# Performance work log

Measured on AMD Instinct MI355X. Metric: run time of the kernel, lower is better.

Reference implementation:

```python
import jax, jax.numpy as jnp
import numpy as np
from jax import lax

PART = 224   # PART_IMAGE_SIZE
PAD = 224    # PAD_SIZE
TOPN = 4
IOU_THRESH = 0.25
N_ANCHORS = 1614


def _conv(x, w, b, stride, pad):
    y = lax.conv_general_dilated(x, w, (stride, stride), [(pad, pad), (pad, pad)],
                                 dimension_numbers=('NCHW', 'OIHW', 'NCHW'))
    return y + b[None, :, None, None]


def _iou(box, boxes):
    # box [4], boxes [N,4] as (y0,x0,y1,x1)
    yy0 = jnp.maximum(box[0], boxes[:, 0]); xx0 = jnp.maximum(box[1], boxes[:, 1])
    yy1 = jnp.minimum(box[2], boxes[:, 2]); xx1 = jnp.minimum(box[3], boxes[:, 3])
    inter = jnp.clip(yy1 - yy0, 0.0) * jnp.clip(xx1 - xx0, 0.0)
    a = (box[2] - box[0]) * (box[3] - box[1])
    areas = (boxes[:, 2] - boxes[:, 0]) * (boxes[:, 3] - boxes[:, 1])
    return inter / (a + areas - inter)


def _nms(scores, boxes):
    # hard NMS keeping TOPN boxes; returns indices [TOPN]
    valid = jnp.ones(scores.shape, dtype=bool)
    idxs = []
    for _ in range(TOPN):
        i = jnp.argmax(jnp.where(valid, scores, -jnp.inf))
        idxs.append(i)
        valid = valid & (_iou(boxes[i], boxes) <= IOU_THRESH)
    return jnp.stack(idxs)


def _crop_resize(img, box):
    # img [3,Hp,Wp] padded image, box [4] float; bilinear, align_corners=True,
    # matching F.interpolate(x_pad[:, :, y0:y1, x0:x1], (PART, PART))
    Hp, Wp = img.shape[1], img.shape[2]
    def coords(c0, c1, L):
        t = jnp.arange(PART, dtype=img.dtype) / (PART - 1)
        c = c0 + (c1 - 1.0 - c0) * t          # absolute source coordinate
        cf = jnp.floor(c)
        lo = jnp.clip(cf.astype(jnp.int32), 0, L - 1)
        hi = jnp.clip(lo + 1, 0, L - 1)
        return lo, hi, c - cf
    yl, yh, wy = coords(box[0], box[2], Hp)
    xl, xh, wx = coords(box[1], box[3], Wp)
    g = lambda yi, xi: img[:, yi[:, None], xi[None, :]]   # [3,PART,PART]
    return ((1 - wy)[:, None] * ((1 - wx) * g(yl, xl) + wx * g(yl, xh))
            + wy[:, None] * ((1 - wx) * g(yh, xl) + wx * g(yh, xh)))


def setup_inputs() -> dict:
    key = jax.random.key(0)
    ks = jax.random.split(key, 20)
    x = jax.random.uniform(ks[0], (16, 3, 448, 448), dtype=jnp.float32)
    rpn_feature = jax.random.normal(ks[1], (16, 2048, 14, 14), dtype=jnp.float32)
    # valid boxes inside the padded 896x896 image
    y0 = jax.random.randint(ks[2], (N_ANCHORS,), 0, 560)
    x0 = jax.random.randint(ks[3], (N_ANCHORS,), 0, 560)
    h = jax.random.randint(ks[4], (N_ANCHORS,), 32, 336)
    w = jax.random.randint(ks[5], (N_ANCHORS,), 32, 336)
    anchors = jnp.stack([y0, x0, jnp.minimum(y0 + h, 896), jnp.minimum(x0 + w, 896)], axis=1).astype(jnp.int32)
    s = 0.02
    inp = {
        'x': x, 'rpn_feature': rpn_feature, 'anchors': anchors,
        'w_down1': jax.random.normal(ks[6], (128, 2048, 3, 3), jnp.float32) * s,
        'b_down1': jnp.zeros((128,), jnp.float32),
        'w_down2': jax.random.normal(ks[7], (128, 128, 3, 3), jnp.float32) * s,
        'b_down2': jnp.zeros((128,), jnp.float32),
        'w_down3': jax.random.normal(ks[8], (128, 128, 3, 3), jnp.float32) * s,
        'b_down3': jnp.zeros((128,), jnp.float32),
        'w_tidy1': jax.random.normal(ks[9], (6, 128, 1, 1), jnp.float32) * s,
        'b_tidy1': jnp.zeros((6,), jnp.float32),
        'w_tidy2': jax.random.normal(ks[10], (6, 128, 1, 1), jnp.float32) * s,
        'b_tidy2': jnp.zeros((6,), jnp.float32),
        'w_tidy3': jax.random.normal(ks[11], (9, 128, 1, 1), jnp.float32) * s,
        'b_tidy3': jnp.zeros((9,), jnp.float32),
    }
    return inp


def reference(x, rpn_feature, anchors,
              w_down1, b_down1, w_down2, b_down2, w_down3, b_down3,
              w_tidy1, b_tidy1, w_tidy2, b_tidy2, w_tidy3, b_tidy3):
    B = x.shape[0]
    # ProposalNet
    d1 = jax.nn.relu(_conv(rpn_feature, w_down1, b_down1, 1, 1))   # [B,128,14,14]
    d2 = jax.nn.relu(_conv(d1, w_down2, b_down2, 2, 1))            # [B,128,7,7]
    d3 = jax.nn.relu(_conv(d2, w_down3, b_down3, 2, 1))            # [B,128,4,4]
    t1 = _conv(d1, w_tidy1, b_tidy1, 1, 0).reshape(B, -1)
    t2 = _conv(d2, w_tidy2, b_tidy2, 1, 0).reshape(B, -1)
    t3 = _conv(d3, w_tidy3, b_tidy3, 1, 0).reshape(B, -1)
    rpn_score = jnp.concatenate([t1, t2, t3], axis=1)              # [B, 1614]
    boxes = anchors.astype(x.dtype)                                # [N,4]
    top_n_index = jax.vmap(lambda s: _nms(s, boxes))(rpn_score)    # [B,TOPN]
    top_n_prob = jnp.take_along_axis(rpn_score, top_n_index, axis=1)
    x_pad = jnp.pad(x, ((0, 0), (0, 0), (PAD, PAD), (PAD, PAD)))   # [B,3,896,896]
    sel_boxes = boxes[top_n_index]                                 # [B,TOPN,4]
    part_imgs = jax.vmap(lambda img, bxs: jax.vmap(lambda b: _crop_resize(img, b))(bxs))(x_pad, sel_boxes)
    # part_imgs: [B,TOPN,3,PART,PART]
    return rpn_score, top_n_index, top_n_prob, part_imgs
```

## Files before the change

kernel.cpp:

```cpp
#include <hip/hip_runtime.h>
#include <hip/hip_bf16.h>

#define NB 16
#define NA 1614
#define NBP (NB * 196 * 128)

typedef __bf16 bf16x8 __attribute__((ext_vector_type(8)));
typedef float f32x4 __attribute__((ext_vector_type(4)));

__device__ __forceinline__ unsigned short f2bf(float v) {
  unsigned u = __float_as_uint(v);
  unsigned r = (u + 0x7FFFu + ((u >> 16) & 1u)) >> 16;
  return (unsigned short)r;
}
__device__ __forceinline__ float bf2f(unsigned short s) {
  return __uint_as_float(((unsigned)s) << 16);
}

__global__ __launch_bounds__(256)
void prep(const float* __restrict__ w, const float* __restrict__ in,
          unsigned short* __restrict__ wTh, unsigned short* __restrict__ wTl,
          unsigned short* __restrict__ aTh, unsigned short* __restrict__ aTl) {
  __shared__ float s[32 * 201];
  const int bid = blockIdx.x;
  if (bid < 1024) {
    const int chunk = bid & 63, b = bid >> 6;
    const float* src = in + ((size_t)b * 2048 + chunk * 32) * 196;
#pragma unroll
    for (int r = 0; r < 7; r++) {
      int e = threadIdx.x + 256 * r;
      if (e < 1568) {
        int ic = e / 49, f = e - ic * 49;
        float4 v = ((const float4*)(src + (size_t)ic * 196))[f];
        float* d = s + ic * 201 + f * 4;
        d[0] = v.x; d[1] = v.y; d[2] = v.z; d[3] = v.w;
      }
    }
    __syncthreads();
    unsigned short* oh = aTh + (size_t)bid * (196 * 32);
    unsigned short* ol = aTl + (size_t)bid * (196 * 32);
#pragma unroll
    for (int r = 0; r < 4; r++) {
      int e = threadIdx.x + 256 * r;
      if (e < 784) {
        int pos = e >> 2, part = e & 3;
        unsigned short hv[8], lv[8];
#pragma unroll
        for (int j = 0; j < 8; j++) {
          float v = s[(part * 8 + j) * 201 + pos];
          unsigned short h = f2bf(v);
          hv[j] = h;
          lv[j] = f2bf(v - bf2f(h));
        }
        ((uint4*)oh)[e] = *(uint4*)hv;
        ((uint4*)ol)[e] = *(uint4*)lv;
      }
    }
  } else {
    int e = (bid - 1024) * 256 + threadIdx.x;
    if (e < 9 * 128 * 2048) {
      int tap = e / (128 * 2048);
      int rem = e - tap * (128 * 2048);
      int oc = rem >> 11, ic = rem & 2047;
      float v = w[((size_t)oc * 2048 + ic) * 9 + tap];
      unsigned short h = f2bf(v);
      wTh[e] = h;
      wTl[e] = f2bf(v - bf2f(h));
    }
  }
}

__global__ __launch_bounds__(256, 3)
void conv1_mfma(const unsigned short* __restrict__ aTh, const unsigned short* __restrict__ aTl,
                const unsigned short* __restrict__ wTh, const unsigned short* __restrict__ wTl,
                float* __restrict__ p1) {
  const int bid = blockIdx.x;
  const int b  = bid & 15;
  const int nh = (bid >> 4) & 1;
  const int kc = bid >> 5;
  const int tid = threadIdx.x;
  const int wid = tid >> 6, lane = tid & 63;
  const int wm = wid & 1, wn = wid >> 1;
  const int q = lane >> 4, ln = lane & 15;

  __shared__ unsigned short sAh[4 * 2048];
  __shared__ unsigned short sAl[4 * 2048];
  __shared__ unsigned short sBh[4 * 512];
  __shared__ unsigned short sBl[4 * 512];

  for (int e = tid; e < 4096; e += 256) {
    ((unsigned int*)sAh)[e] = 0u;
    ((unsigned int*)sAl)[e] = 0u;
  }

  int abase[7];
#pragma unroll
  for (int mf = 0; mf < 7; mf++) {
    int row = wm * 112 + mf * 16 + ln;
    int y = row / 14, x = row - y * 14;
    abase[mf] = ((row < 196) ? (y * 16 + x) : 0) * 8;
  }
  const int qoff = q * 2048;

  f32x4 acc[7][2];
#pragma unroll
  for (int mf = 0; mf < 7; mf++)
#pragma unroll
    for (int nf = 0; nf < 2; nf++) acc[mf][nf] = (f32x4){0.f, 0.f, 0.f, 0.f};

  const int boc = tid >> 2, bicq = tid & 3;
  const size_t bocbase = (size_t)(nh * 64 + boc) << 11;

  uint4 pvh, pvl;
  {
    size_t g = bocbase + kc * 128 + bicq * 8;
    pvh = *(const uint4*)(wTh + g);
    pvl = *(const uint4*)(wTl + g);
  }

  for (int it = 0; it < 36; it++) {
    const int ks = it / 9, tap = it - ks * 9;
    __syncthreads();
    *(uint4*)(sBh + bicq * 512 + boc * 8) = pvh;
    *(uint4*)(sBl + bicq * 512 + boc * 8) = pvl;
    if (tap == 0) {
      const uint4* gh = (const uint4*)(aTh + ((size_t)(b * 64 + kc * 4 + ks) * 196) * 32);
      const uint4* gl = (const uint4*)(aTl + ((size_t)(b * 64 + kc * 4 + ks) * 196) * 32);
#pragma unroll
      for (int r = 0; r < 4; r++) {
        int e = tid + 256 * r;
        if (e < 784) {
          int pos = e >> 2, part = e & 3;
          int py = pos / 14, px = pos - py * 14;
          int dst = part * 2048 + ((py + 1) * 16 + px + 1) * 8;
          *(uint4*)(sAh + dst) = gh[e];
          *(uint4*)(sAl + dst) = gl[e];
        }
      }
    }
    {
      const int nit = (it < 35) ? it + 1 : 35;
      const int ks2 = nit / 9, tap2 = nit - ks2 * 9;
      size_t g = (size_t)tap2 * (128 * 2048) + bocbase + kc * 128 + ks2 * 32 + bicq * 8;
      pvh = *(const uint4*)(wTh + g);
      pvl = *(const uint4*)(wTl + g);
    }
    __syncthreads();

    const int t8 = ((tap / 3) * 16 + (tap % 3)) * 8;
    bf16x8 bh[2], bl[2];
#pragma unroll
    for (int nf = 0; nf < 2; nf++) {
      const int bb = q * 512 + (wn * 32 + nf * 16 + ln) * 8;
      bh[nf] = *(const bf16x8*)(sBh + bb);
      bl[nf] = *(const bf16x8*)(sBl + bb);
    }
#pragma unroll
    for (int mf = 0; mf < 7; mf++) {
      bf16x8 ah = *(const bf16x8*)(sAh + qoff + abase[mf] + t8);
      bf16x8 al = *(const bf16x8*)(sAl + qoff + abase[mf] + t8);
#pragma unroll
      for (int nf = 0; nf < 2; nf++) {
        acc[mf][nf] = __builtin_amdgcn_mfma_f32_16x16x32_bf16(ah, bh[nf], acc[mf][nf], 0, 0, 0);
        acc[mf][nf] = __builtin_amdgcn_mfma_f32_16x16x32_bf16(al, bh[nf], acc[mf][nf], 0, 0, 0);
        acc[mf][nf] = __builtin_amdgcn_mfma_f32_16x16x32_bf16(ah, bl[nf], acc[mf][nf], 0, 0, 0);
      }
    }
  }

  float* pk = p1 + ((size_t)kc * NB + b) * 196 * 128;
#pragma unroll
  for (int mf = 0; mf < 7; mf++) {
    const int row0 = wm * 112 + mf * 16 + q * 4;
#pragma unroll
    for (int nf = 0; nf < 2; nf++) {
      const int oc = nh * 64 + wn * 32 + nf * 16 + ln;
#pragma unroll
      for (int r = 0; r < 4; r++) {
        const int row = row0 + r;
        if (row < 196) pk[(size_t)row * 128 + oc] = acc[mf][nf][r];
      }
    }
  }
}

__global__ __launch_bounds__(256)
void conv1_finish_p(const float* __restrict__ p1, const float* __restrict__ bias,
                    float* __restrict__ d1) {
  __shared__ float s[28 * 132];
  const int bid = blockIdx.x;
  const int pt = bid % 7, b = bid / 7;
  const int tid = threadIdx.x;
#pragma unroll
  for (int r = 0; r < 4; r++) {
    int u = tid + 256 * r;
    if (u < 896) {
      int pos = u >> 5, oc4 = u & 31;
      const float* base = p1 + ((size_t)(b * 196 + pt * 28 + pos)) * 128 + oc4 * 4;
      float4 sum = ((const float4*)bias)[oc4];
#pragma unroll
      for (int k = 0; k < 16; k++) {
        float4 v = *(const float4*)(base + (size_t)k * NBP);
        sum.x += v.x; sum.y += v.y; sum.z += v.z; sum.w += v.w;
      }
      sum.x = fmaxf(sum.x, 0.f); sum.y = fmaxf(sum.y, 0.f);
      sum.z = fmaxf(sum.z, 0.f); sum.w = fmaxf(sum.w, 0.f);
      *(float4*)(s + pos * 132 + oc4 * 4) = sum;
    }
  }
  __syncthreads();
#pragma unroll
  for (int r = 0; r < 4; r++) {
    int u = tid + 256 * r;
    if (u < 896) {
      int oc = u / 7, f = u - oc * 7;
      float4 v;
      v.x = s[(f * 4 + 0) * 132 + oc];
      v.y = s[(f * 4 + 1) * 132 + oc];
      v.z = s[(f * 4 + 2) * 132 + oc];
      v.w = s[(f * 4 + 3) * 132 + oc];
      *(float4*)(d1 + ((size_t)b * 128 + oc) * 196 + pt * 28 + f * 4) = v;
    }
  }
}

__global__ void conv2_part(const float* __restrict__ d1, const float* __restrict__ w,
                           float* __restrict__ p2) {
  const int bid = blockIdx.x;
  const int kc = bid & 3, oct = (bid >> 2) & 3, b = bid >> 4;
  const int ic0 = kc * 32, oc0 = oct * 32;
  const int tid = threadIdx.x;
  const int ocl = tid >> 3, rw = tid & 7;

  __shared__ float s_in[32 * 320];
  __shared__ float s_w[32 * 324];

#pragma unroll
  for (int r = 0; r < 32; r++) {
    const int e = tid + 256 * r;
    const int ch = e >> 8, idx = e & 255;
    const int tr = idx >> 4, tc = idx & 15;
    const int iy = tr - 1, ix = tc - 1;
    float v = 0.f;
    if ((unsigned)iy < 14u && (unsigned)ix < 14u)
      v = d1[((size_t)b * 128 + ic0 + ch) * 196 + iy * 14 + ix];
    s_in[ch * 320 + tr * 20 + tc] = v;
  }
#pragma unroll
  for (int r = 0; r < 36; r++) {
    const int e = tid + 256 * r;
    const int oc = e / 288, rem = e - oc * 288;
    const int ch = rem / 9, tap = rem - ch * 9;
    s_w[ch * 324 + tap * 36 + oc] =
        w[(size_t)(oc0 + oc) * 1152 + (size_t)ic0 * 9 + rem];
  }
  __syncthreads();

  if (rw < 7) {
    float acc[7] = {};
    for (int ic = 0; ic < 32; ic++) {
      const float* wrow = s_w + ic * 324 + ocl;
      const float* irow = s_in + ic * 320;
#pragma unroll
      for (int ky = 0; ky < 3; ky++) {
        const float* r = irow + (2 * rw + ky) * 20;
        const float4 f0 = *(const float4*)(r);
        const float4 f1 = *(const float4*)(r + 4);
        const float4 f2 = *(const float4*)(r + 8);
        const float4 f3 = *(const float4*)(r + 12);
        const float ev[8] = {f0.x, f0.z, f1.x, f1.z, f2.x, f2.z, f3.x, f3.z};
        const float od[7] = {f0.y, f0.w, f1.y, f1.w, f2.y, f2.w, f3.y};
        const float w0 = wrow[(ky * 3 + 0) * 36];
        const float w1 = wrow[(ky * 3 + 1) * 36];
        const float w2 = wrow[(ky * 3 + 2) * 36];
#pragma unroll
        for (int x = 0; x < 7; x++)
          acc[x] = fmaf(w0, ev[x], fmaf(w1, od[x], fmaf(w2, ev[x + 1], acc[x])));
      }
    }
    float* po = p2 + (((size_t)kc * NB + b) * 128 + oc0 + ocl) * 49 + rw * 7;
#pragma unroll
    for (int x = 0; x < 7; x++) po[x] = acc[x];
  }
}

__global__ void conv2_finish(const float* __restrict__ p2, const float* __restrict__ bias,
                             float* __restrict__ d2) {
  const int i = blockIdx.x * 256 + threadIdx.x;
  if (i >= NB * 128 * 49) return;
  const int oc = (i / 49) & 127;
  float s = bias[oc];
#pragma unroll
  for (int k = 0; k < 4; k++) s += p2[(size_t)k * (NB * 128 * 49) + i];
  d2[i] = fmaxf(s, 0.f);
}

__global__ void conv3_part(const float* __restrict__ d2, const float* __restrict__ w,
                           float* __restrict__ p3) {
  const int bid = blockIdx.x;
  const int kc = bid & 1, oct = (bid >> 1) & 7, b = bid >> 4;
  const int ic0 = kc * 64, oc0 = oct * 16;
  const int tid = threadIdx.x;
  const int oc = tid >> 4, p = tid & 15;
  const int y = p >> 2, x = p & 3;

  __shared__ float s_in[64 * 108];
  __shared__ float s_w[64 * 144];

#pragma unroll
  for (int r = 0; r < 21; r++) {
    const int e = tid + 256 * r;
    if (e < 64 * 81) {
      const int ch = e / 81, idx = e - ch * 81;
      const int tr = idx / 9, tc = idx - tr * 9;
      const int iy = tr - 1, ix = tc - 1;
      float v = 0.f;
      if ((unsigned)iy < 7u && (unsigned)ix < 7u)
        v = d2[((size_t)b * 128 + ic0 + ch) * 49 + iy * 7 + ix];
      s_in[ch * 108 + tr * 12 + tc] = v;
    }
  }
#pragma unroll
  for (int r = 0; r < 36; r++) {
    const int e = tid + 256 * r;
    const int o = e / 576, rem = e - o * 576;
    const int ch = rem / 9, tap = rem - ch * 9;
    s_w[ch * 144 + tap * 16 + o] =
        w[(size_t)(oc0 + o) * 1152 + (size_t)ic0 * 9 + rem];
  }
  __syncthreads();

  float acc = 0.f;
  for (int ic = 0; ic < 64; ic++) {
    const float* wrow = s_w + ic * 144 + oc;
    const float* irow = s_in + ic * 108 + 2 * y * 12 + 2 * x;
#pragma unroll
    for (int ky = 0; ky < 3; ky++)
#pragma unroll
      for (int kx = 0; kx < 3; kx++)
        acc = fmaf(wrow[(ky * 3 + kx) * 16], irow[ky * 12 + kx], acc);
  }
  p3[(((size_t)kc * NB + b) * 128 + oc0 + oc) * 16 + p] = acc;
}

__global__ __launch_bounds__(256, 1)
void score_nms(const float* __restrict__ d1, const float* __restrict__ d2,
               const float* __restrict__ p3, const float* __restrict__ bd3,
               const float* __restrict__ w1, const float* __restrict__ b1,
               const float* __restrict__ w2, const float* __restrict__ b2,
               const float* __restrict__ w3, const float* __restrict__ b3,
               const int* __restrict__ anchors, float* __restrict__ score,
               float* __restrict__ out_idx, float* __restrict__ out_prob,
               float* __restrict__ sel) {
  __shared__ float s_in[32 * 200];
  __shared__ float s_w[21 * 128];
  __shared__ float s_b[21];
  __shared__ float s_sc[NA];
  __shared__ float s_bx[NA * 4];
  __shared__ float r_s[256];
  __shared__ int r_i[256];
  const int b = blockIdx.x, tid = threadIdx.x;

  for (int i = tid; i < 768; i += 256) s_w[i] = w1[i];
  for (int i = tid; i < 768; i += 256) s_w[768 + i] = w2[i];
  for (int i = tid; i < 1152; i += 256) s_w[1536 + i] = w3[i];
  if (tid < 21) s_b[tid] = (tid < 6) ? b1[tid] : (tid < 12) ? b2[tid - 6] : b3[tid - 12];
  for (int i = tid; i < NA; i += 256) {
    s_bx[i * 4 + 0] = (float)anchors[i * 4 + 0];
    s_bx[i * 4 + 1] = (float)anchors[i * 4 + 1];
    s_bx[i * 4 + 2] = (float)anchors[i * 4 + 2];
    s_bx[i * 4 + 3] = (float)anchors[i * 4 + 3];
  }

  float acc[5] = {0.f, 0.f, 0.f, 0.f, 0.f};
  for (int chunk = 0; chunk < 4; chunk++) {
    __syncthreads();
    const float* src = d1 + ((size_t)b * 128 + chunk * 32) * 196;
#pragma unroll
    for (int r = 0; r < 7; r++) {
      int e = tid + 256 * r;
      if (e < 1568) {
        int ic = e / 49, f = e - ic * 49;
        *(float4*)(s_in + ic * 200 + f * 4) = ((const float4*)(src + (size_t)ic * 196))[f];
      }
    }
    __syncthreads();
#pragma unroll
    for (int k = 0; k < 5; k++) {
      int j = tid + 256 * k;
      if (j < 1176) {
        int oc = j / 196, p = j - oc * 196;
        const float* wr = s_w + oc * 128 + chunk * 32;
        float s = acc[k];
#pragma unroll
        for (int ic = 0; ic < 32; ic++) s = fmaf(wr[ic], s_in[ic * 200 + p], s);
        acc[k] = s;
      }
    }
  }
#pragma unroll
  for (int k = 0; k < 5; k++) {
    int j = tid + 256 * k;
    if (j < 1176) {
      int oc = j / 196;
      float s = acc[k] + s_b[oc];
      s_sc[j] = s;
      score[b * NA + j] = s;
    }
  }

  __syncthreads();
  {
    const float* src = d2 + (size_t)b * 6272;
#pragma unroll
    for (int r = 0; r < 7; r++) {
      int e = tid + 256 * r;
      if (e < 1568) *(float4*)(s_in + e * 4) = ((const float4*)src)[e];
    }
  }
  __syncthreads();
#pragma unroll
  for (int k = 0; k < 2; k++) {
    int jj = tid + 256 * k;
    if (jj < 294) {
      int oc = jj / 49, p = jj - oc * 49;
      const float* wr = s_w + 768 + oc * 128;
      float s = s_b[6 + oc];
#pragma unroll 8
      for (int ic = 0; ic < 128; ic++) s = fmaf(wr[ic], s_in[ic * 49 + p], s);
      s_sc[1176 + jj] = s;
      score[b * NA + 1176 + jj] = s;
    }
  }

  __syncthreads();
  {
    const float4* s0 = (const float4*)(p3 + (size_t)b * 2048);
    const float4* s1 = (const float4*)(p3 + 32768 + (size_t)b * 2048);
#pragma unroll
    for (int r = 0; r < 2; r++) {
      int e = tid + 256 * r;
      if (e < 512) {
        float4 a = s0[e], c = s1[e];
        float bb = bd3[e >> 2];
        float4 v;
        v.x = fmaxf(a.x + c.x + bb, 0.f);
        v.y = fmaxf(a.y + c.y + bb, 0.f);
        v.z = fmaxf(a.z + c.z + bb, 0.f);
        v.w = fmaxf(a.w + c.w + bb, 0.f);
        *(float4*)(s_in + e * 4) = v;
      }
    }
  }
  __syncthreads();
  if (tid < 144) {
    int oc = tid >> 4, p = tid & 15;
    const float* wr = s_w + 1536 + oc * 128;
    float s = s_b[12 + oc];
#pragma unroll 8
    for (int ic = 0; ic < 128; ic++) s = fmaf(wr[ic], s_in[ic * 16 + p], s);
    s_sc[1470 + tid] = s;
    score[b * NA + 1470 + tid] = s;
  }
  __syncthreads();

  for (int t = 0; t < 4; t++) {
    float bs = -__builtin_inff();
    int bi = NA;
    for (int i = tid; i < NA; i += 256) {
      float s = s_sc[i];
      if (s > bs || (s == bs && i < bi)) { bs = s; bi = i; }
    }
    r_s[tid] = bs; r_i[tid] = bi;
    __syncthreads();
    for (int off = 128; off > 0; off >>= 1) {
      if (tid < off) {
        float s2 = r_s[tid + off]; int i2 = r_i[tid + off];
        if (s2 > r_s[tid] || (s2 == r_s[tid] && i2 < r_i[tid])) { r_s[tid] = s2; r_i[tid] = i2; }
      }
      __syncthreads();
    }
    const int idx = r_i[0];
    const float by0 = s_bx[idx * 4 + 0], bx0 = s_bx[idx * 4 + 1];
    const float by1 = s_bx[idx * 4 + 2], bx1 = s_bx[idx * 4 + 3];
    if (tid == 0) {
      out_idx[b * 4 + t] = (float)idx;
      out_prob[b * 4 + t] = s_sc[idx];
      sel[(b * 4 + t) * 4 + 0] = by0;
      sel[(b * 4 + t) * 4 + 1] = bx0;
      sel[(b * 4 + t) * 4 + 2] = by1;
      sel[(b * 4 + t) * 4 + 3] = bx1;
    }
    __syncthreads();
    const float a = (by1 - by0) * (bx1 - bx0);
    for (int i = tid; i < NA; i += 256) {
      float cy0 = s_bx[i * 4 + 0], cx0 = s_bx[i * 4 + 1];
      float cy1 = s_bx[i * 4 + 2], cx1 = s_bx[i * 4 + 3];
      float yy0 = fmaxf(by0, cy0), xx0 = fmaxf(bx0, cx0);
      float yy1 = fminf(by1, cy1), xx1 = fminf(bx1, cx1);
      float inter = fmaxf(yy1 - yy0, 0.f) * fmaxf(xx1 - xx0, 0.f);
      float ar = (cy1 - cy0) * (cx1 - cx0);
      float iou = inter / (a + ar - inter);
      if (iou > 0.25f) s_sc[i] = -__builtin_inff();
    }
    __syncthreads();
  }
}

__global__ void crop_kernel(const float* __restrict__ x, const float* __restrict__ sel,
                            float* __restrict__ out) {
  int i4 = blockIdx.x * 256 + threadIdx.x;
  const int total4 = NB * 4 * 3 * 224 * 56;
  if (i4 >= total4) return;
  int px0 = (i4 % 56) * 4;
  int t = i4 / 56;
  int py = t % 224; t /= 224;
  int ch = t % 3;  t /= 3;
  int n  = t % 4;
  int b  = t / 4;

  const float* bx = sel + (b * 4 + n) * 4;
  const float y0 = bx[0], x0 = bx[1], y1 = bx[2], x1 = bx[3];

  float ty = (float)py / 223.0f;
  float cy = y0 + (y1 - 1.0f - y0) * ty;
  float cyf = floorf(cy);
  int ylo = (int)cyf; ylo = ylo < 0 ? 0 : (ylo > 895 ? 895 : ylo);
  int yhi = ylo + 1 > 895 ? 895 : ylo + 1;
  float wy = cy - cyf;

  const float* img = x + ((size_t)b * 3 + ch) * 448 * 448;
  auto g = [&](int yy, int xx) -> float {
    yy -= 224; xx -= 224;
    if ((unsigned)yy < 448u && (unsigned)xx < 448u)
      return img[(size_t)yy * 448 + xx];
    return 0.f;
  };

  float4 res;
  float* rp = &res.x;
#pragma unroll
  for (int k = 0; k < 4; k++) {
    float tx = (float)(px0 + k) / 223.0f;
    float cx = x0 + (x1 - 1.0f - x0) * tx;
    float cxf = floorf(cx);
    int xlo = (int)cxf; xlo = xlo < 0 ? 0 : (xlo > 895 ? 895 : xlo);
    int xhi = xlo + 1 > 895 ? 895 : xlo + 1;
    float wx = cx - cxf;
    float v00 = g(ylo, xlo), v01 = g(ylo, xhi);
    float v10 = g(yhi, xlo), v11 = g(yhi, xhi);
    rp[k] = (1.f - wy) * ((1.f - wx) * v00 + wx * v01) +
            wy * ((1.f - wx) * v10 + wx * v11);
  }
  *(float4*)(out + (size_t)i4 * 4) = res;
}

extern "C" void kernel_launch(void* const* d_in, const int* in_sizes, int n_in,
                              void* d_out, int out_size, void* d_ws, size_t ws_size,
                              hipStream_t stream) {
  const float* x    = (const float*)d_in[0];
  const float* rpn  = (const float*)d_in[1];
  const int*   anc  = (const int*)d_in[2];
  const float* w_d1 = (const float*)d_in[3];
  const float* b_d1 = (const float*)d_in[4];
  const float* w_d2 = (const float*)d_in[5];
  const float* b_d2 = (const float*)d_in[6];
  const float* w_d3 = (const float*)d_in[7];
  const float* b_d3 = (const float*)d_in[8];
  const float* w_t1 = (const float*)d_in[9];
  const float* b_t1 = (const float*)d_in[10];
  const float* w_t2 = (const float*)d_in[11];
  const float* b_t2 = (const float*)d_in[12];
  const float* w_t3 = (const float*)d_in[13];
  const float* b_t3 = (const float*)d_in[14];

  float* out = (float*)d_out;
  float* ws = (float*)d_ws;

  float* d1  = ws;
  float* d2  = d1 + 401408;
  float* d3  = d2 + 100352;
  float* sel = d3 + 32768;
  float* p2  = sel + 256;
  float* p3  = p2 + 401408;
  unsigned short* wTh = (unsigned short*)(p3 + 65536);
  unsigned short* wTl = wTh + 2359296;
  unsigned short* aTh = wTl + 2359296;
  unsigned short* aTl = aTh + 6422528;

  float* score    = out;
  float* out_idx  = out + 25824;
  float* out_prob = out + 25888;
  float* parts    = out + 25952;
  float* p1       = parts;

  prep<<<dim3(10240), dim3(256), 0, stream>>>(w_d1, rpn, wTh, wTl, aTh, aTl);
  conv1_mfma<<<dim3(512), dim3(256), 0, stream>>>(aTh, aTl, wTh, wTl, p1);
  conv1_finish_p<<<dim3(112), dim3(256), 0, stream>>>(p1, b_d1, d1);
  conv2_part<<<dim3(256), dim3(256), 0, stream>>>(d1, w_d2, p2);
  conv2_finish<<<dim3(392), dim3(256), 0, stream>>>(p2, b_d2, d2);
  conv3_part<<<dim3(256), dim3(256), 0, stream>>>(d2, w_d3, p3);
  score_nms<<<dim3(16), dim3(256), 0, stream>>>(d1, d2, p3, b_d3, w_t1, b_t1, w_t2, b_t2,
                                                w_t3, b_t3, anc, score, out_idx, out_prob, sel);
  crop_kernel<<<dim3(9408), dim3(256), 0, stream>>>(x, sel, parts);
}
```

Before: 282.1 us.

## Widen conv1 MFMA tile to all 128 output channels per block

Each conv1 block now computes all 128 output channels instead of a 64-channel half, so the activation tile loaded into shared memory is reused across twice as many MFMAs and the grid halves to 256 blocks. Shared-memory row strides are padded (2064/1040) to reduce bank conflicts, and the next-weight prefetch moves after the barrier. Launch bounds drop to one block per SM to allow the doubled accumulator set, which reduces occupancy and latency hiding, and 256 blocks may underfill the device's compute units.

After: 285.9 us. About the same (+1.4%).

```diff
diff --git a/kernel.cpp b/kernel.cpp
--- a/kernel.cpp
+++ b/kernel.cpp
@@ -70,25 +70,24 @@
   }
 }
 
-__global__ __launch_bounds__(256, 3)
+__global__ __launch_bounds__(256, 1)
 void conv1_mfma(const unsigned short* __restrict__ aTh, const unsigned short* __restrict__ aTl,
                 const unsigned short* __restrict__ wTh, const unsigned short* __restrict__ wTl,
                 float* __restrict__ p1) {
   const int bid = blockIdx.x;
-  const int b  = bid & 15;
-  const int nh = (bid >> 4) & 1;
-  const int kc = bid >> 5;
+  const int kc = bid & 15;
+  const int b  = bid >> 4;
   const int tid = threadIdx.x;
   const int wid = tid >> 6, lane = tid & 63;
   const int wm = wid & 1, wn = wid >> 1;
   const int q = lane >> 4, ln = lane & 15;
 
-  __shared__ unsigned short sAh[4 * 2048];
-  __shared__ unsigned short sAl[4 * 2048];
-  __shared__ unsigned short sBh[4 * 512];
-  __shared__ unsigned short sBl[4 * 512];
-
-  for (int e = tid; e < 4096; e += 256) {
+  __shared__ unsigned short sAh[4 * 2064];
+  __shared__ unsigned short sAl[4 * 2064];
+  __shared__ unsigned short sBh[4 * 1040];
+  __shared__ unsigned short sBl[4 * 1040];
+
+  for (int e = tid; e < 4128; e += 256) {
     ((unsigned int*)sAh)[e] = 0u;
     ((unsigned int*)sAl)[e] = 0u;
   }
@@ -100,29 +99,34 @@
     int y = row / 14, x = row - y * 14;
     abase[mf] = ((row < 196) ? (y * 16 + x) : 0) * 8;
   }
-  const int qoff = q * 2048;
-
-  f32x4 acc[7][2];
+  const int qoff = q * 2064;
+
+  f32x4 acc[7][4];
 #pragma unroll
   for (int mf = 0; mf < 7; mf++)
 #pragma unroll
-    for (int nf = 0; nf < 2; nf++) acc[mf][nf] = (f32x4){0.f, 0.f, 0.f, 0.f};
+    for (int nf = 0; nf < 4; nf++) acc[mf][nf] = (f32x4){0.f, 0.f, 0.f, 0.f};
 
   const int boc = tid >> 2, bicq = tid & 3;
-  const size_t bocbase = (size_t)(nh * 64 + boc) << 11;
-
-  uint4 pvh, pvl;
+  const size_t bocbase0 = (size_t)boc << 11;
+  const size_t bocbase1 = (size_t)(boc + 64) << 11;
+
+  uint4 pvh0, pvl0, pvh1, pvl1;
   {
-    size_t g = bocbase + kc * 128 + bicq * 8;
-    pvh = *(const uint4*)(wTh + g);
-    pvl = *(const uint4*)(wTl + g);
+    const size_t g = (size_t)kc * 128 + bicq * 8;
+    pvh0 = *(const uint4*)(wTh + g + bocbase0);
+    pvl0 = *(const uint4*)(wTl + g + bocbase0);
+    pvh1 = *(const uint4*)(wTh + g + bocbase1);
+    pvl1 = *(const uint4*)(wTl + g + bocbase1);
   }
 
   for (int it = 0; it < 36; it++) {
     const int ks = it / 9, tap = it - ks * 9;
     __syncthreads();
-    *(uint4*)(sBh + bicq * 512 + boc * 8) = pvh;
-    *(uint4*)(sBl + bicq * 512 + boc * 8) = pvl;
+    *(uint4*)(sBh + bicq * 1040 + boc * 8) = pvh0;
+    *(uint4*)(sBl + bicq * 1040 + boc * 8) = pvl0;
+    *(uint4*)(sBh + bicq * 1040 + boc * 8 + 512) = pvh1;
+    *(uint4*)(sBl + bicq * 1040 + boc * 8 + 512) = pvl1;
     if (tap == 0) {
       const uint4* gh = (const uint4*)(aTh + ((size_t)(b * 64 + kc * 4 + ks) * 196) * 32);
       const uint4* gl = (const uint4*)(aTl + ((size_t)(b * 64 + kc * 4 + ks) * 196) * 32);
@@ -132,26 +136,28 @@
         if (e < 784) {
           int pos = e >> 2, part = e & 3;
           int py = pos / 14, px = pos - py * 14;
-          int dst = part * 2048 + ((py + 1) * 16 + px + 1) * 8;
+          int dst = part * 2064 + ((py + 1) * 16 + px + 1) * 8;
           *(uint4*)(sAh + dst) = gh[e];
           *(uint4*)(sAl + dst) = gl[e];
         }
       }
     }
+    __syncthreads();
     {
       const int nit = (it < 35) ? it + 1 : 35;
       const int ks2 = nit / 9, tap2 = nit - ks2 * 9;
-      size_t g = (size_t)tap2 * (128 * 2048) + bocbase + kc * 128 + ks2 * 32 + bicq * 8;
-      pvh = *(const uint4*)(wTh + g);
-      pvl = *(const uint4*)(wTl + g);
-    }
-    __syncthreads();
+      const size_t g = (size_t)tap2 * (128 * 2048) + kc * 128 + ks2 * 32 + bicq * 8;
+      pvh0 = *(const uint4*)(wTh + g + bocbase0);
+      pvl0 = *(const uint4*)(wTl + g + bocbase0);
+      pvh1 = *(const uint4*)(wTh + g + bocbase1);
+      pvl1 = *(const uint4*)(wTl + g + bocbase1);
+    }
 
     const int t8 = ((tap / 3) * 16 + (tap % 3)) * 8;
-    bf16x8 bh[2], bl[2];
-#pragma unroll
-    for (int nf = 0; nf < 2; nf++) {
-      const int bb = q * 512 + (wn * 32 + nf * 16 + ln) * 8;
+    bf16x8 bh[4], bl[4];
+#pragma unroll
+    for (int nf = 0; nf < 4; nf++) {
+      const int bb = q * 1040 + (wn * 64 + nf * 16 + ln) * 8;
       bh[nf] = *(const bf16x8*)(sBh + bb);
       bl[nf] = *(const bf16x8*)(sBl + bb);
     }
@@ -160,7 +166,7 @@
       bf16x8 ah = *(const bf16x8*)(sAh + qoff + abase[mf] + t8);
       bf16x8 al = *(const bf16x8*)(sAl + qoff + abase[mf] + t8);
 #pragma unroll
-      for (int nf = 0; nf < 2; nf++) {
+      for (int nf = 0; nf < 4; nf++) {
         acc[mf][nf] = __builtin_amdgcn_mfma_f32_16x16x32_bf16(ah, bh[nf], acc[mf][nf], 0, 0, 0);
         acc[mf][nf] = __builtin_amdgcn_mfma_f32_16x16x32_bf16(al, bh[nf], acc[mf][nf], 0, 0, 0);
         acc[mf][nf] = __builtin_amdgcn_mfma_f32_16x16x32_bf16(ah, bl[nf], acc[mf][nf], 0, 0, 0);
@@ -173,8 +179,8 @@
   for (int mf = 0; mf < 7; mf++) {
     const int row0 = wm * 112 + mf * 16 + q * 4;
 #pragma unroll
-    for (int nf = 0; nf < 2; nf++) {
-      const int oc = nh * 64 + wn * 32 + nf * 16 + ln;
+    for (int nf = 0; nf < 4; nf++) {
+      const int oc = wn * 64 + nf * 16 + ln;
 #pragma unroll
       for (int r = 0; r < 4; r++) {
         const int row = row0 + r;
@@ -595,7 +601,7 @@
   float* p1       = parts;
 
   prep<<<dim3(10240), dim3(256), 0, stream>>>(w_d1, rpn, wTh, wTl, aTh, aTl);
-  conv1_mfma<<<dim3(512), dim3(256), 0, stream>>>(aTh, aTl, wTh, wTl, p1);
+  conv1_mfma<<<dim3(256), dim3(256), 0, stream>>>(aTh, aTl, wTh, wTl, p1);
   conv1_finish_p<<<dim3(112), dim3(256), 0, stream>>>(p1, b_d1, d1);
   conv2_part<<<dim3(256), dim3(256), 0, stream>>>(d1, w_d2, p2);
   conv2_finish<<<dim3(392), dim3(256), 0, stream>>>(p2, b_d2, d2);
```
